# Performance work log

Hardware: AMD Instinct MI355X
Metric: run time of the kernel (lower is better)

Reference implementation:

```python
import jax, jax.numpy as jnp
import numpy as np

DIM = 1024
HEADS = 16
HEAD_DIM = DIM // HEADS
RANK = 16
ALPHA = 8.0
SCALING = ALPHA / RANK  # 0.5
SCALE = HEAD_DIM ** (-0.5)
B_, L_ = 2, 2048


def _proj_params(key, std=0.02):
    kW, kb, kA, kB = jax.random.split(key, 4)
    W = jax.random.normal(kW, (DIM, DIM), jnp.float32) * std   # [out, in]
    b = jax.random.normal(kb, (DIM,), jnp.float32) * std
    A = jax.random.normal(kA, (DIM, RANK), jnp.float32) * std  # [out, r]
    Bm = jax.random.normal(kB, (RANK, DIM), jnp.float32) * std # [r, in]
    return W, b, A, Bm


def setup_inputs() -> dict:
    key = jax.random.key(0)
    ks = jax.random.split(key, 6)
    x = jax.random.normal(ks[0], (B_, L_, DIM), jnp.float32)
    attn_bias = jax.random.normal(ks[1], (1, HEADS, L_, L_), jnp.float32) * 0.1
    inp = {"x": x, "attn_bias": attn_bias}
    for name, k in zip("qkvo", ks[2:6]):
        W, b, A, Bm = _proj_params(k)
        inp[f"W{name}"] = W
        inp[f"b{name}"] = b
        inp[f"A{name}"] = A
        inp[f"B{name}"] = Bm
    return inp


def _lora_linear(x, W, b, A, Bm):
    # y = x W^T + b + scaling * ((x @ A) @ B)   (matches torch LoRALinear)
    return x @ W.T + b + SCALING * ((x @ A) @ Bm)


def _split(x):
    B, L, D = x.shape
    return jnp.swapaxes(x.reshape(B, L, HEADS, HEAD_DIM), 1, 2)  # [B,H,L,hd]


def reference(x, attn_bias, Wq, bq, Aq, Bq, Wk, bk, Ak, Bk, Wv, bv, Av, Bv, Wo, bo, Ao, Bo):
    B, L, D = x.shape
    q = _split(_lora_linear(x, Wq, bq, Aq, Bq))
    k = _split(_lora_linear(x, Wk, bk, Ak, Bk))
    v = _split(_lora_linear(x, Wv, bv, Av, Bv))
    scores = jnp.einsum('bhld,bhmd->bhlm', q, k) * SCALE + attn_bias
    attn = jax.nn.softmax(scores, axis=-1)  # dropout p=0 -> identity
    out = jnp.einsum('bhlm,bhmd->bhld', attn, v)
    out = jnp.swapaxes(out, 1, 2).reshape(B, L, D)  # merge heads
    return _lora_linear(out, Wo, bo, Ao, Bo)
```

## Files before the change

kernel.cpp:

```cpp
#include <hip/hip_runtime.h>
#include <cstdint>

typedef __bf16 bf16;
typedef __bf16 bf16x8 __attribute__((ext_vector_type(8)));
typedef __bf16 bf16x4 __attribute__((ext_vector_type(4)));
typedef float  f32x4  __attribute__((ext_vector_type(4)));
typedef float  f32x16 __attribute__((ext_vector_type(16)));
typedef int    i32x4  __attribute__((ext_vector_type(4)));

#define DIM   1024
#define LSEQ  2048
#define NH    16
#define HD    64
#define NTOK  4096

#define AS1C(p) ((const __attribute__((address_space(1))) void*)(unsigned long long)(uintptr_t)(p))
#define AS3P(p) ((__attribute__((address_space(3))) void*)(unsigned int)(uintptr_t)(p))
#define SB0 __builtin_amdgcn_sched_barrier(0)

__device__ __forceinline__ f32x4 mfma16(bf16x8 a, bf16x8 b, f32x4 c) {
  return __builtin_amdgcn_mfma_f32_16x16x32_bf16(a, b, c, 0, 0, 0);
}
__device__ __forceinline__ f32x16 mfma32(bf16x8 a, bf16x8 b, f32x16 c) {
  return __builtin_amdgcn_mfma_f32_32x32x16_bf16(a, b, c, 0, 0, 0);
}
__device__ __forceinline__ int pk2(float a, float b) {
  unsigned short ua = __builtin_bit_cast(unsigned short, (bf16)a);
  unsigned short ub = __builtin_bit_cast(unsigned short, (bf16)b);
  return (int)ua | ((int)ub << 16);
}

__global__ __launch_bounds__(256) void k_cvt(const float* __restrict__ x,
                                             bf16* __restrict__ xb) {
  const int i = (blockIdx.x * 256 + threadIdx.x) * 4;
  const f32x4 v = *(const f32x4*)(x + i);
  bf16x4 o;
  o[0] = (bf16)v[0]; o[1] = (bf16)v[1]; o[2] = (bf16)v[2]; o[3] = (bf16)v[3];
  *(bf16x4*)(xb + i) = o;
}

struct WeffArgs {
  const float* W[4]; const float* A[4]; const float* B[4]; bf16* out[4];
};

__global__ __launch_bounds__(256) void k_weff(WeffArgs args) {
  const int o = blockIdx.x;
  const int z = blockIdx.y;
  const float* __restrict__ W  = args.W[z];
  const float* __restrict__ A  = args.A[z];
  const float* __restrict__ Bm = args.B[z];
  bf16* __restrict__ out = args.out[z];
  float Bo[16];
#pragma unroll
  for (int r = 0; r < 16; ++r) Bo[r] = Bm[r * DIM + o];
#pragma unroll
  for (int j = 0; j < 4; ++j) {
    const int d = j * 256 + (int)threadIdx.x;
    const float* Ar = A + (size_t)d * 16;
    float acc = 0.f;
#pragma unroll
    for (int r = 0; r < 16; ++r) acc += Ar[r] * Bo[r];
    out[(size_t)o * DIM + d] = (bf16)(W[(size_t)o * DIM + d] + 0.5f * acc);
  }
}

template <int NF, bool F32OUT>
__device__ __forceinline__ void gemm_body64(const bf16* __restrict__ X,
                                            const bf16* __restrict__ W,
                                            const float* __restrict__ bias,
                                            void* __restrict__ out,
                                            float scale, int m0, int n0, int ncol0) {
  constexpr int BN = NF * 32;
  constexpr int BJ = BN / 32;
  __shared__ __align__(16) bf16 As[128 * 64];
  __shared__ __align__(16) bf16 Bs[BN * 64];
  const int tid  = threadIdx.x;
  const int lane = tid & 63, w = tid >> 6;
  const int l15 = lane & 15, l4 = lane >> 4;
  const int wr = w >> 1, wc = w & 1;
  const int lr = lane >> 3;
  const int scol = ((lane & 7) ^ lr) * 8;

  f32x4 acc[4][NF] = {};
  const bf16* ag = X + (size_t)m0 * DIM;
  const bf16* bg = W + (size_t)n0 * DIM;

  for (int kt = 0; kt < DIM / 64; ++kt) {
    const int k0 = kt * 64;
#pragma unroll
    for (int j = 0; j < 4; ++j) {
      const int rb = w * 4 + j;
      __builtin_amdgcn_global_load_lds(
          AS1C(ag + (size_t)(rb * 8 + lr) * DIM + k0 + scol),
          AS3P(As + rb * 512), 16, 0, 0);
    }
#pragma unroll
    for (int j = 0; j < BJ; ++j) {
      const int rb = w * BJ + j;
      __builtin_amdgcn_global_load_lds(
          AS1C(bg + (size_t)(rb * 8 + lr) * DIM + k0 + scol),
          AS3P(Bs + rb * 512), 16, 0, 0);
    }
    __syncthreads();
    bf16x8 af[2][4], bfr[2][NF];
#pragma unroll
    for (int ks = 0; ks < 2; ++ks) {
#pragma unroll
      for (int m = 0; m < 4; ++m) {
        const int r = wr * 64 + m * 16 + l15;
        af[ks][m] = *(const bf16x8*)(As + r * 64 + ((ks * 4 + l4) ^ (r & 7)) * 8);
      }
#pragma unroll
      for (int n = 0; n < NF; ++n) {
        const int r = wc * (NF * 16) + n * 16 + l15;
        bfr[ks][n] = *(const bf16x8*)(Bs + r * 64 + ((ks * 4 + l4) ^ (r & 7)) * 8);
      }
    }
#pragma unroll
    for (int m = 0; m < 4; ++m)
#pragma unroll
      for (int n = 0; n < NF; ++n) {
        acc[m][n] = mfma16(af[0][m], bfr[0][n], acc[m][n]);
        acc[m][n] = mfma16(af[1][m], bfr[1][n], acc[m][n]);
      }
    __syncthreads();
  }

#pragma unroll
  for (int m = 0; m < 4; ++m) {
    const int r0 = m0 + wr * 64 + m * 16 + l4 * 4;
#pragma unroll
    for (int n = 0; n < NF; ++n) {
      const int c = ncol0 + wc * (NF * 16) + n * 16 + l15;
      const float bc = bias[c];
#pragma unroll
      for (int t = 0; t < 4; ++t) {
        const float y = (acc[m][n][t] + bc) * scale;
        if constexpr (F32OUT)
          ((float*)out)[(size_t)(r0 + t) * DIM + c] = y;
        else
          ((bf16*)out)[(size_t)(r0 + t) * DIM + c] = (bf16)y;
      }
    }
  }
}

__global__ __launch_bounds__(256) void k_gemm_qkv(
    const bf16* __restrict__ xb, const bf16* __restrict__ weff,
    const float* __restrict__ bq, const float* __restrict__ bk,
    const float* __restrict__ bv,
    bf16* __restrict__ q, bf16* __restrict__ k, bf16* __restrict__ v) {
  const int n0 = blockIdx.y * 128;
  const int z = n0 >> 10;
  const float* bias = (z == 0) ? bq : (z == 1) ? bk : bv;
  bf16* out = (z == 0) ? q : (z == 1) ? k : v;
  const float scale = (z == 0) ? 0.125f : 1.0f;
  gemm_body64<4, false>(xb, weff, bias, out, scale, blockIdx.x * 128, n0, n0 & 1023);
}

__global__ __launch_bounds__(256) void k_gemm_o(
    const bf16* __restrict__ ctx, const bf16* __restrict__ weffo,
    const float* __restrict__ bo, float* __restrict__ out) {
  const int n0 = blockIdx.y * 64;
  gemm_body64<2, true>(ctx, weffo, bo, out, 1.0f, blockIdx.x * 128, n0, n0);
}

__global__ __launch_bounds__(256) void k_vfrag(const bf16* __restrict__ v,
                                               const bf16* __restrict__ k,
                                               bf16* __restrict__ vf,
                                               bf16* __restrict__ kf) {
  const int lt = blockIdx.x, bh = blockIdx.y;
  const int b = bh >> 4, h = bh & 15;
  __shared__ __align__(16) bf16 tile[64][72];
  const int tid = threadIdx.x;
  const int r = tid >> 2, c0 = (tid & 3) * 16;
  const bf16* src = v + (size_t)(b * LSEQ + lt * 64) * DIM + h * HD;
  *(bf16x8*)(&tile[r][c0])     = *(const bf16x8*)(src + (size_t)r * DIM + c0);
  *(bf16x8*)(&tile[r][c0 + 8]) = *(const bf16x8*)(src + (size_t)r * DIM + c0 + 8);
  __syncthreads();
  const int w = tid >> 6, lane = tid & 63, l31 = lane & 31, hi = lane >> 5;
  {
    const int tt = w >> 1, n = w & 1;
    const int t = lt * 2 + tt;
#pragma unroll
    for (int c = 0; c < 2; ++c) {
      bf16 tmp[8];
#pragma unroll
      for (int j = 0; j < 8; ++j)
        tmp[j] = tile[tt * 32 + c * 16 + hi * 8 + j][n * 32 + l31];
      *(bf16x8*)(vf + ((((size_t)bh * 64 + t) * 4 + n * 2 + c) * 64 + lane) * 8) =
          *(bf16x8*)tmp;
    }
  }
  {
    const int t = lt * 2 + (w & 1);
    const bf16* krow = k + (size_t)(b * LSEQ + t * 32 + l31) * DIM + h * HD + hi * 8;
#pragma unroll
    for (int cc = 0; cc < 2; ++cc) {
      const int c = (w >> 1) + cc * 2;
      *(bf16x8*)(kf + ((((size_t)bh * 64 + t) * 4 + c) * 64 + lane) * 8) =
          *(const bf16x8*)(krow + c * 16);
    }
  }
}

__global__ __launch_bounds__(512, 1) void k_attn(
    const bf16* __restrict__ q, const bf16* __restrict__ kf,
    const bf16* __restrict__ vf, const float* __restrict__ bias,
    bf16* __restrict__ ctx) {
  const int tid = threadIdx.x, w = tid >> 6, lane = tid & 63;
  const int l31 = lane & 31, hi = lane >> 5;
  const int bb = w >> 2, qs = w & 3;
  const int h = blockIdx.x & 15;
  const int q0 = (blockIdx.x >> 4) * 128;

  __shared__ __align__(16) bf16  kls[2][4][2048];
  __shared__ __align__(16) bf16  vls[2][4][2048];
  __shared__ __align__(16) float bls[4][4096];

  const bf16* qrow = q + (size_t)(bb * LSEQ + q0 + qs * 32 + l31) * DIM + h * HD;
  bf16x8 Qf[4];
#pragma unroll
  for (int c = 0; c < 4; ++c) Qf[c] = *(const bf16x8*)(qrow + c * 16 + hi * 8);

  const int kvA = 2 * w, kvB = 2 * w + 1;
  const int kbA = kvA >> 3, vvA = (kvA >> 2) & 1, cA = kvA & 3;
  const int kbB = kvB >> 3, vvB = (kvB >> 2) & 1, cB = kvB & 3;
  const bf16* srcA = (vvA ? vf : kf) + (size_t)(kbA * NH + h) * 64 * 2048 + cA * 512 + lane * 8;
  const bf16* srcB = (vvB ? vf : kf) + (size_t)(kbB * NH + h) * 64 * 2048 + cB * 512 + lane * 8;
  bf16* dstA = (vvA ? &vls[kbA][0][0] : &kls[kbA][0][0]) + cA * 512 + lane * 8;
  bf16* dstB = (vvB ? &vls[kbB][0][0] : &kls[kbB][0][0]) + cB * 512 + lane * 8;
  const int lr = lane >> 3, lc = lane & 7;
  const float* bsA = bias + ((size_t)h * LSEQ + q0 + 16 * w + lr) * LSEQ + 4 * (lc ^ lr);
  const float* bsB = bsA + (size_t)8 * LSEQ;
  float* bdA = &bls[0][0] + (2 * w) * 256 + lane * 4;
  float* bdB = bdA + 256;

  f32x16 acc0 = {}, acc1 = {};
  float mrun = -3e38f, lrun = 0.f;

#define STAGE(t_, s_)                                                          \
  {                                                                            \
    __builtin_amdgcn_global_load_lds(AS1C(srcA + (size_t)(t_) * 2048),         \
                                     AS3P(dstA + (s_) * 2048), 16, 0, 0);      \
    __builtin_amdgcn_global_load_lds(AS1C(srcB + (size_t)(t_) * 2048),         \
                                     AS3P(dstB + (s_) * 2048), 16, 0, 0);      \
    __builtin_amdgcn_global_load_lds(AS1C(bsA + (size_t)(t_) * 32),            \
                                     AS3P(bdA + (s_) * 4096), 16, 0, 0);       \
    __builtin_amdgcn_global_load_lds(AS1C(bsB + (size_t)(t_) * 32),            \
                                     AS3P(bdB + (s_) * 4096), 16, 0, 0);       \
  }

  STAGE(0, 0); SB0;
  STAGE(1, 1); SB0;
  STAGE(2, 2); SB0;

  const int rr = qs * 32 + l31;
  const int sw = (l31 & 7) << 2;
  for (int t = 0; t < 64; ++t) {
    const int sl = t & 3;
    const int tn = (t + 3 > 63) ? 63 : t + 3;
    STAGE(tn, (t + 3) & 3); SB0;
    asm volatile("s_waitcnt vmcnt(12)" ::: "memory");
    __builtin_amdgcn_s_barrier();

    bf16x8 Kf[4], Vf[2][2];
    f32x4 br[4];
#pragma unroll
    for (int c = 0; c < 4; ++c)
      Kf[c] = *(const bf16x8*)(&kls[bb][sl][c * 512 + lane * 8]);
#pragma unroll
    for (int u = 0; u < 4; ++u)
      Vf[u >> 1][u & 1] = *(const bf16x8*)(&vls[bb][sl][u * 512 + lane * 8]);
#pragma unroll
    for (int g = 0; g < 4; ++g)
      br[g] = *(const f32x4*)(
          &bls[sl][rr * 32 + (((g << 3) | (hi << 2)) ^ sw)]);
    asm volatile("s_waitcnt lgkmcnt(0)" ::: "memory");
    SB0;
    __builtin_amdgcn_s_barrier();

    f32x16 s = {};
#pragma unroll
    for (int c = 0; c < 4; ++c) s = mfma32(Kf[c], Qf[c], s);
    float p[16];
#pragma unroll
    for (int r = 0; r < 16; ++r) p[r] = s[r] + br[r >> 2][r & 3];
    float m8[8];
#pragma unroll
    for (int i = 0; i < 8; ++i) m8[i] = fmaxf(p[i], p[i + 8]);
    float tm = fmaxf(fmaxf(fmaxf(m8[0], m8[4]), fmaxf(m8[1], m8[5])),
                     fmaxf(fmaxf(m8[2], m8[6]), fmaxf(m8[3], m8[7])));
    tm = fmaxf(tm, __shfl_xor(tm, 32));
    if (!__all(tm <= mrun + 8.0f)) {
      const float mn = fmaxf(mrun, tm);
      const float scl = __expf(mrun - mn);
      mrun = mn;
      lrun *= scl;
#pragma unroll
      for (int r = 0; r < 16; ++r) { acc0[r] *= scl; acc1[r] *= scl; }
    }
#pragma unroll
    for (int r = 0; r < 16; ++r) p[r] = __expf(p[r] - mrun);
    float s8[8];
#pragma unroll
    for (int i = 0; i < 8; ++i) s8[i] = p[i] + p[i + 8];
    float rs = ((s8[0] + s8[1]) + (s8[2] + s8[3])) + ((s8[4] + s8[5]) + (s8[6] + s8[7]));
    rs += __shfl_xor(rs, 32);
    lrun += rs;
#pragma unroll
    for (int c = 0; c < 2; ++c) {
      const int c8 = c * 8;
      const int A0 = pk2(p[c8 + 0], p[c8 + 1]);
      const int A1 = pk2(p[c8 + 2], p[c8 + 3]);
      const int B0 = pk2(p[c8 + 4], p[c8 + 5]);
      const int B1 = pk2(p[c8 + 6], p[c8 + 7]);
      const int pA0 = __shfl_xor(A0, 32), pA1 = __shfl_xor(A1, 32);
      const int pB0 = __shfl_xor(B0, 32), pB1 = __shfl_xor(B1, 32);
      i32x4 fi;
      fi[0] = hi ? pB0 : A0;
      fi[1] = hi ? pB1 : A1;
      fi[2] = hi ? B0 : pA0;
      fi[3] = hi ? B1 : pA1;
      const bf16x8 pf = __builtin_bit_cast(bf16x8, fi);
      acc0 = mfma32(Vf[0][c], pf, acc0);
      acc1 = mfma32(Vf[1][c], pf, acc1);
    }
  }
#undef STAGE

  const float inv = 1.0f / lrun;
  bf16* cp = ctx + (size_t)(bb * LSEQ + q0 + qs * 32 + l31) * DIM + h * HD;
#pragma unroll
  for (int r = 0; r < 16; ++r) {
    const int dr = (r & 3) + 8 * (r >> 2) + 4 * hi;
    cp[dr]      = (bf16)(acc0[r] * inv);
    cp[32 + dr] = (bf16)(acc1[r] * inv);
  }
}

extern "C" void kernel_launch(void* const* d_in, const int* in_sizes, int n_in,
                              void* d_out, int out_size, void* d_ws, size_t ws_size,
                              hipStream_t stream) {
  const float* x  = (const float*)d_in[0];
  const float* ab = (const float*)d_in[1];
  const float* Wq = (const float*)d_in[2];  const float* bq = (const float*)d_in[3];
  const float* Aq = (const float*)d_in[4];  const float* Bq = (const float*)d_in[5];
  const float* Wk = (const float*)d_in[6];  const float* bk = (const float*)d_in[7];
  const float* Ak = (const float*)d_in[8];  const float* Bk = (const float*)d_in[9];
  const float* Wv = (const float*)d_in[10]; const float* bv = (const float*)d_in[11];
  const float* Av = (const float*)d_in[12]; const float* Bv = (const float*)d_in[13];
  const float* Wo = (const float*)d_in[14]; const float* bo = (const float*)d_in[15];
  const float* Ao = (const float*)d_in[16]; const float* Bo = (const float*)d_in[17];

  uint8_t* ws = (uint8_t*)d_ws;
  const size_t SZ = (size_t)NTOK * DIM * sizeof(bf16);
  bf16* xb   = (bf16*)(ws + 0 * SZ);
  bf16* weff = (bf16*)(ws + 1 * SZ);
  bf16* qb   = (bf16*)(ws + 2 * SZ);
  bf16* kb   = (bf16*)(ws + 3 * SZ);
  bf16* vb   = (bf16*)(ws + 4 * SZ);
  bf16* kfb  = (bf16*)(ws + 5 * SZ);
  bf16* vfb  = (bf16*)(ws + 6 * SZ);
  bf16* ctx  = (bf16*)(ws + 7 * SZ);

  k_cvt<<<dim3(NTOK * DIM / 1024), 256, 0, stream>>>(x, xb);

  WeffArgs wa;
  wa.W[0] = Wq; wa.A[0] = Aq; wa.B[0] = Bq; wa.out[0] = weff;
  wa.W[1] = Wk; wa.A[1] = Ak; wa.B[1] = Bk; wa.out[1] = weff + (size_t)DIM * DIM;
  wa.W[2] = Wv; wa.A[2] = Av; wa.B[2] = Bv; wa.out[2] = weff + 2 * (size_t)DIM * DIM;
  wa.W[3] = Wo; wa.A[3] = Ao; wa.B[3] = Bo; wa.out[3] = weff + 3 * (size_t)DIM * DIM;
  k_weff<<<dim3(DIM, 4), 256, 0, stream>>>(wa);

  k_gemm_qkv<<<dim3(32, 24), 256, 0, stream>>>(xb, weff, bq, bk, bv, qb, kb, vb);
  k_vfrag<<<dim3(32, 32), 256, 0, stream>>>(vb, kb, vfb, kfb);
  k_attn<<<dim3(256), 512, 0, stream>>>(qb, kfb, vfb, ab, ctx);
  k_gemm_o<<<dim3(32, 16), 256, 0, stream>>>(ctx, weff + 3 * (size_t)DIM * DIM, bo,
                                             (float*)d_out);
}
```

Measured before the change: 170.3 us.

## Load K/V fragments directly from global into registers, double-buffered

K and V tiles are no longer staged through LDS with global_load_lds. Each wave now reads its pre-swizzled K/V fragments straight from global memory into registers, ping-ponging between two register sets across an unrolled-by-two loop, while only the attention bias still goes through LDS. This removes LDS traffic and LDS capacity for K/V and the ds_read step, at the cost of more VGPRs, redundant global reads by the four waves sharing a batch, and fragile vmcnt bookkeeping now that the number of in-flight loads has changed.

```diff
diff --git a/kernel.cpp b/kernel.cpp
--- a/kernel.cpp
+++ b/kernel.cpp
@@ -214,8 +214,6 @@
   const int h = blockIdx.x & 15;
   const int q0 = (blockIdx.x >> 4) * 128;
 
-  __shared__ __align__(16) bf16  kls[2][4][2048];
-  __shared__ __align__(16) bf16  vls[2][4][2048];
   __shared__ __align__(16) float bls[4][4096];
 
   const bf16* qrow = q + (size_t)(bb * LSEQ + q0 + qs * 32 + l31) * DIM + h * HD;
@@ -223,13 +221,9 @@
 #pragma unroll
   for (int c = 0; c < 4; ++c) Qf[c] = *(const bf16x8*)(qrow + c * 16 + hi * 8);
 
-  const int kvA = 2 * w, kvB = 2 * w + 1;
-  const int kbA = kvA >> 3, vvA = (kvA >> 2) & 1, cA = kvA & 3;
-  const int kbB = kvB >> 3, vvB = (kvB >> 2) & 1, cB = kvB & 3;
-  const bf16* srcA = (vvA ? vf : kf) + (size_t)(kbA * NH + h) * 64 * 2048 + cA * 512 + lane * 8;
-  const bf16* srcB = (vvB ? vf : kf) + (size_t)(kbB * NH + h) * 64 * 2048 + cB * 512 + lane * 8;
-  bf16* dstA = (vvA ? &vls[kbA][0][0] : &kls[kbA][0][0]) + cA * 512 + lane * 8;
-  bf16* dstB = (vvB ? &vls[kbB][0][0] : &kls[kbB][0][0]) + cB * 512 + lane * 8;
+  const bf16* kvK = kf + (size_t)(bb * NH + h) * 64 * 2048 + lane * 8;
+  const bf16* kvV = vf + (size_t)(bb * NH + h) * 64 * 2048 + lane * 8;
+
   const int lr = lane >> 3, lc = lane & 7;
   const float* bsA = bias + ((size_t)h * LSEQ + q0 + 16 * w + lr) * LSEQ + 4 * (lc ^ lr);
   const float* bsB = bsA + (size_t)8 * LSEQ;
@@ -238,40 +232,28 @@
 
   f32x16 acc0 = {}, acc1 = {};
   float mrun = -3e38f, lrun = 0.f;
-
-#define STAGE(t_, s_)                                                          \
+  bf16x8 KA[4], KB[4], VA[2][2], VB[2][2];
+
+#define BSTAGE(t_, s_)                                                         \
   {                                                                            \
-    __builtin_amdgcn_global_load_lds(AS1C(srcA + (size_t)(t_) * 2048),         \
-                                     AS3P(dstA + (s_) * 2048), 16, 0, 0);      \
-    __builtin_amdgcn_global_load_lds(AS1C(srcB + (size_t)(t_) * 2048),         \
-                                     AS3P(dstB + (s_) * 2048), 16, 0, 0);      \
     __builtin_amdgcn_global_load_lds(AS1C(bsA + (size_t)(t_) * 32),            \
                                      AS3P(bdA + (s_) * 4096), 16, 0, 0);       \
     __builtin_amdgcn_global_load_lds(AS1C(bsB + (size_t)(t_) * 32),            \
                                      AS3P(bdB + (s_) * 4096), 16, 0, 0);       \
   }
-
-  STAGE(0, 0); SB0;
-  STAGE(1, 1); SB0;
-  STAGE(2, 2); SB0;
+#define LOADKV(K_, V_, t_)                                                     \
+  {                                                                            \
+    _Pragma("unroll") for (int c_ = 0; c_ < 4; ++c_)                           \
+        K_[c_] = *(const bf16x8*)(kvK + ((t_) * 4 + c_) * 512);                \
+    _Pragma("unroll") for (int u_ = 0; u_ < 4; ++u_)                           \
+        V_[u_ >> 1][u_ & 1] = *(const bf16x8*)(kvV + ((t_) * 4 + u_) * 512);   \
+  }
 
   const int rr = qs * 32 + l31;
   const int sw = (l31 & 7) << 2;
-  for (int t = 0; t < 64; ++t) {
-    const int sl = t & 3;
-    const int tn = (t + 3 > 63) ? 63 : t + 3;
-    STAGE(tn, (t + 3) & 3); SB0;
-    asm volatile("s_waitcnt vmcnt(12)" ::: "memory");
-    __builtin_amdgcn_s_barrier();
-
-    bf16x8 Kf[4], Vf[2][2];
+
+  auto step = [&](const bf16x8 (&Kf)[4], const bf16x8 (&Vf)[2][2], int sl) {
     f32x4 br[4];
-#pragma unroll
-    for (int c = 0; c < 4; ++c)
-      Kf[c] = *(const bf16x8*)(&kls[bb][sl][c * 512 + lane * 8]);
-#pragma unroll
-    for (int u = 0; u < 4; ++u)
-      Vf[u >> 1][u & 1] = *(const bf16x8*)(&vls[bb][sl][u * 512 + lane * 8]);
 #pragma unroll
     for (int g = 0; g < 4; ++g)
       br[g] = *(const f32x4*)(
@@ -326,8 +308,27 @@
       acc0 = mfma32(Vf[0][c], pf, acc0);
       acc1 = mfma32(Vf[1][c], pf, acc1);
     }
-  }
-#undef STAGE
+  };
+
+  BSTAGE(0, 0); SB0;
+  BSTAGE(1, 1); SB0;
+  LOADKV(KA, VA, 0); SB0;
+  BSTAGE(2, 2); SB0;
+
+  for (int t = 0; t < 64; t += 2) {
+    LOADKV(KB, VB, t + 1); SB0;
+    { const int tc = (t + 3 > 63) ? 63 : t + 3; BSTAGE(tc, (t + 3) & 3); } SB0;
+    asm volatile("s_waitcnt vmcnt(12)" ::: "memory");
+    __builtin_amdgcn_s_barrier();
+    step(KA, VA, t & 3);
+    { const int tn = (t + 2 > 63) ? 63 : t + 2; LOADKV(KA, VA, tn); } SB0;
+    { const int tc = (t + 4 > 63) ? 63 : t + 4; BSTAGE(tc, (t + 4) & 3); } SB0;
+    asm volatile("s_waitcnt vmcnt(12)" ::: "memory");
+    __builtin_amdgcn_s_barrier();
+    step(KB, VB, (t + 1) & 3);
+  }
+#undef BSTAGE
+#undef LOADKV
 
   const float inv = 1.0f / lrun;
   bf16* cp = ctx + (size_t)(bb * LSEQ + q0 + qs * 32 + l31) * DIM + h * HD;
```

After: 195.7 us. +14.9%, slower.
